# Optimization experiments

Measured on AMD Instinct MI355X. Metric: run time of the kernel, lower is better.

Reference implementation:

```python
import jax, jax.numpy as jnp
from jax import lax
import numpy as np

IMG = 512
NUM_CLASSES = 80
K_PRE = 256            # per-class pre-NMS candidates (TF combined NMS prunes similarly)
MAX_PER_CLASS = 100
MAX_TOTAL = 100
IOU_THR = 0.5
ANY_IOU_THR = 0.7
SCORE_THR = 0.05
NEG = -1e9


def make_anchors(img=IMG):
    """RetinaNet-style anchors for FPN levels 3..7, 9 per cell, [y1,x1,y2,x2]."""
    out = []
    for l in range(3, 8):
        s = 2 ** l
        n = img // s
        c = (np.arange(n) + 0.5) * s
        cy, cx = np.meshgrid(c, c, indexing='ij')
        base = 4.0 * s
        hs, ws = [], []
        for r in [0.5, 1.0, 2.0]:
            for sc in [1.0, 2 ** (1 / 3), 2 ** (2 / 3)]:
                hs.append(base * sc * np.sqrt(r))
                ws.append(base * sc / np.sqrt(r))
        hs = np.asarray(hs); ws = np.asarray(ws)  # [9]
        cy = cy[..., None]; cx = cx[..., None]
        a = np.stack([cy - hs / 2, cx - ws / 2, cy + hs / 2, cx + ws / 2], -1)  # [n,n,9,4]
        out.append(a.reshape(-1, 4))
    return np.concatenate(out, 0).astype(np.float32)


def setup_inputs() -> dict:
    key = jax.random.key(0)
    k1, k2, k3, k4 = jax.random.split(key, 4)
    anchors = jnp.asarray(make_anchors())          # [49104, 4]
    A = anchors.shape[0]
    B = 8
    # logits biased low, mimicking focal-loss bias init; few anchors fire
    y_cls = jax.random.normal(k1, (B, A, NUM_CLASSES), jnp.float32) - 4.0
    y_bbox = jax.random.normal(k2, (B, A, 4), jnp.float32) * 0.1
    orig_hs = jax.random.randint(k3, (B,), 480, 1080).astype(jnp.int32)
    orig_ws = jax.random.randint(k4, (B,), 640, 1920).astype(jnp.int32)
    return {"y_cls": y_cls, "y_bbox": y_bbox, "anchors": anchors,
            "orig_hs": orig_hs, "orig_ws": orig_ws}


def decode_boxes(anchors, rel):
    """bboxes_from_fast_rcnn: anchors [A,4], rel [B,A,4] -> [B,A,4] (y1,x1,y2,x2)."""
    ha = anchors[:, 2] - anchors[:, 0]
    wa = anchors[:, 3] - anchors[:, 1]
    cya = anchors[:, 0] + 0.5 * ha
    cxa = anchors[:, 1] + 0.5 * wa
    cy = cya + rel[..., 0] * ha
    cx = cxa + rel[..., 1] * wa
    h = ha * jnp.exp(rel[..., 2])
    w = wa * jnp.exp(rel[..., 3])
    return jnp.stack([cy - 0.5 * h, cx - 0.5 * w, cy + 0.5 * h, cx + 0.5 * w], -1)


def pairwise_iou(b):
    """[K,4] -> [K,K] IoU."""
    y1, x1, y2, x2 = b[:, 0], b[:, 1], b[:, 2], b[:, 3]
    area = (y2 - y1) * (x2 - x1)
    ih = jnp.maximum(jnp.minimum(y2[:, None], y2[None, :]) - jnp.maximum(y1[:, None], y1[None, :]), 0.0)
    iw = jnp.maximum(jnp.minimum(x2[:, None], x2[None, :]) - jnp.maximum(x1[:, None], x1[None, :]), 0.0)
    inter = ih * iw
    return inter / (area[:, None] + area[None, :] - inter + 1e-8)


def greedy_nms(boxes, valid, iou_thr, max_keep):
    """Greedy NMS over score-sorted boxes [K,4]; returns keep mask [K]."""
    K = boxes.shape[0]
    iou_m = pairwise_iou(boxes)
    ar = jnp.arange(K)

    def step(sup, i):
        k = valid[i] & jnp.logical_not(sup[i])
        sup = sup | (k & (iou_m[i] > iou_thr) & (ar > i))
        return sup, k

    _, keep = lax.scan(step, jnp.zeros(K, bool), ar)
    rank = jnp.cumsum(keep) - 1
    return keep & (rank < max_keep)


def reference(y_cls, y_bbox, anchors, orig_hs, orig_ws):
    B, A, C = y_cls.shape
    scores = jax.nn.sigmoid(y_cls)                 # [B,A,C]
    boxes = decode_boxes(anchors, y_bbox)          # [B,A,4]

    # --- per-class combined NMS ---
    st = jnp.swapaxes(scores, 1, 2)                # [B,C,A]
    top_s, top_i = lax.top_k(st, K_PRE)            # [B,C,K]
    boxes_c = jnp.take_along_axis(boxes[:, None, :, :], top_i[..., None], axis=2)  # [B,C,K,4]
    valid = top_s > SCORE_THR
    keep = jax.vmap(jax.vmap(lambda b, v: greedy_nms(b, v, IOU_THR, MAX_PER_CLASS)))(boxes_c, valid)

    masked = jnp.where(keep, top_s, NEG).reshape(B, -1)           # [B,C*K]
    cls_ids = jnp.broadcast_to(jnp.arange(C, dtype=jnp.float32)[None, :, None],
                               (B, C, K_PRE)).reshape(B, -1)
    boxes_flat = boxes_c.reshape(B, -1, 4)

    sel_s, sel_i = lax.top_k(masked, MAX_TOTAL)    # [B,T]
    sel_valid = sel_s > NEG / 2
    sel_boxes = jnp.take_along_axis(boxes_flat, sel_i[..., None], axis=1)
    sel_cls = jnp.take_along_axis(cls_ids, sel_i, axis=1)
    out_scores = jnp.where(sel_valid, sel_s, 0.0)
    out_boxes = jnp.where(sel_valid[..., None], sel_boxes, 0.0)
    out_cls = jnp.where(sel_valid, sel_cls, 0.0)
    valid_det = jnp.sum(sel_valid, axis=1).astype(jnp.int32)

    # --- resize to original image dims (bboxes_resize) ---
    rh = orig_hs.astype(jnp.float32) / IMG
    rw = orig_ws.astype(jnp.float32) / IMG
    scale = jnp.stack([rh, rw, rh, rw], -1)[:, None, :]
    lim = jnp.stack([orig_hs, orig_ws, orig_hs, orig_ws], -1).astype(jnp.float32)[:, None, :]
    rb = jnp.clip(out_boxes * scale, 0.0, lim)

    # --- class-agnostic second NMS (scores already sorted desc) ---
    v2 = jnp.arange(MAX_TOTAL)[None, :] < valid_det[:, None]
    keep2 = jax.vmap(lambda b, v: greedy_nms(b, v, ANY_IOU_THR, MAX_TOTAL))(rb, v2)

    # compact kept detections to the front (ragged gather in the original)
    perm = jnp.argsort(jnp.logical_not(keep2), axis=1, stable=True)
    fb = jnp.take_along_axis(rb, perm[..., None], axis=1)
    fs = jnp.take_along_axis(out_scores, perm, axis=1)
    fc = jnp.take_along_axis(out_cls, perm, axis=1)
    nv = jnp.sum(keep2, axis=1).astype(jnp.int32)
    m = jnp.arange(MAX_TOTAL)[None, :] < nv[:, None]
    return (jnp.where(m[..., None], fb, 0.0), jnp.where(m, fs, 0.0), jnp.where(m, fc, 0.0), nv)
```

## Files before the change

### kernel.cpp

```cpp
#include <hip/hip_runtime.h>
#include <cstdint>

#define NEGF    (-1.0e9f)
#define THR_PRE (-1.55f)
#define THR_VALID (-2.9444389791664403f)
#define CAP 512
#define FCAP 1024
#define NCLS 80
#define APB 512
#define NSH 96
#define SLOT 20
#define BCAP 512
#define KCAP 128

__device__ __forceinline__ unsigned fkey(float v){
  unsigned b = __float_as_uint(v);
  return b ^ ((b & 0x80000000u) ? 0xFFFFFFFFu : 0x80000000u);
}
__device__ __forceinline__ float fkey_inv(unsigned k){
  unsigned b = (k & 0x80000000u) ? (k ^ 0x80000000u) : ~k;
  return __uint_as_float(b);
}

template<int N, int NT>
__device__ void bitonic_desc(unsigned long long* buf){
  const int tid = threadIdx.x;
  __syncthreads();
  for (int k = 2; k <= N; k <<= 1){
    for (int j = k >> 1; j > 0; j >>= 1){
      for (int t = tid; t < N/2; t += NT){
        int i = ((t & ~(j-1)) << 1) | (t & (j-1));
        int p = i | j;
        unsigned long long a = buf[i], b = buf[p];
        bool sw = ((i & k) == 0) ? (a < b) : (a > b);
        if (sw){ buf[i] = b; buf[p] = a; }
      }
      __syncthreads();
    }
  }
}

__global__ void k_filter(const float* __restrict__ ycls, int A,
                         unsigned* __restrict__ pcnt, unsigned long long* __restrict__ pairs){
  const int b  = blockIdx.y;
  const int sh = blockIdx.x;
  const int a0 = sh * APB;
  const int tid = threadIdx.x;
  __shared__ unsigned long long s_cand[BCAP];
  __shared__ unsigned char     s_crow[BCAP];
  __shared__ unsigned s_n;
  __shared__ unsigned s_cnt[NCLS], s_cur[NCLS];
  if (tid == 0) s_n = 0;
  if (tid < NCLS){ s_cnt[tid] = 0u; s_cur[tid] = 0u; }
  __syncthreads();

  const float4* p4 = (const float4*)(ycls + ((size_t)b*A + a0)*NCLS);
  const int nval = (min(APB, A - a0)) * NCLS;
  const int n4 = nval >> 2;
  for (int t = tid; t < n4; t += blockDim.x){
    float4 v = p4[t];
    int idx  = t << 2;
    int aloc = idx / NCLS;
    int c0   = idx - aloc*NCLS;
    unsigned a = (unsigned)(a0 + aloc);
    float vv[4] = {v.x, v.y, v.z, v.w};
    #pragma unroll
    for (int j = 0; j < 4; j++){
      if (vv[j] > THR_PRE){
        unsigned s = atomicAdd(&s_n, 1u);
        if (s < BCAP){
          s_cand[s] = ((unsigned long long)fkey(vv[j]) << 32) | (unsigned)(~a);
          s_crow[s] = (unsigned char)(c0 + j);
        }
      }
    }
  }
  __syncthreads();
  unsigned n = s_n; if (n > BCAP) n = BCAP;
  for (unsigned i = tid; i < n; i += blockDim.x)
    atomicAdd(&s_cnt[s_crow[i]], 1u);
  __syncthreads();
  if (tid < NCLS){
    unsigned ccl = s_cnt[tid]; if (ccl > SLOT) ccl = SLOT;
    pcnt[(size_t)(b*NCLS + tid)*NSH + sh] = ccl;
  }
  for (unsigned i = tid; i < n; i += blockDim.x){
    int c = s_crow[i];
    unsigned off = atomicAdd(&s_cur[c], 1u);
    if (off < SLOT)
      pairs[((size_t)(b*NCLS + c)*NSH + sh)*SLOT + off] = s_cand[i];
  }
}

__global__ void k_topk_nms(const unsigned* __restrict__ pcnt, const unsigned long long* __restrict__ pairs,
                           const float* __restrict__ ycls, const float4* __restrict__ ybbox,
                           const float4* __restrict__ anchors,
                           float4* __restrict__ sbox,
                           unsigned long long* __restrict__ bcand, unsigned* __restrict__ kcnt,
                           unsigned A, unsigned C){
  const int row = blockIdx.x, tid = threadIdx.x;
  const unsigned b = (unsigned)row / C, c = (unsigned)row % C;
  __shared__ __align__(16) char smem[5120];
  unsigned long long* L = (unsigned long long*)smem;
  __shared__ unsigned sc[128];
  __shared__ unsigned s_n, s_kc;
  __shared__ unsigned long long s_K, s_keep[4];

  unsigned ct = 0;
  if (tid < 128){
    ct = (tid < NSH) ? pcnt[(size_t)row*NSH + tid] : 0u;
    sc[tid] = ct;
  }
  __syncthreads();
  #pragma unroll
  for (int d = 1; d < 128; d <<= 1){
    unsigned v = 0;
    if (tid < 128 && tid >= d) v = sc[tid - d];
    __syncthreads();
    if (tid < 128 && tid >= d) sc[tid] += v;
    __syncthreads();
  }
  unsigned n = sc[127];

  for (int i = tid; i < CAP; i += 256) L[i] = 0ull;
  __syncthreads();
  if (n >= 256u){
    if (tid < NSH && ct > 0){
      unsigned base = sc[tid] - ct;
      const unsigned long long* src = pairs + ((size_t)row*NSH + tid)*SLOT;
      for (unsigned i = 0; i < ct; ++i){
        unsigned d = base + i;
        if (d < CAP) L[d] = src[i];
      }
    }
  } else {
    if (tid == 0) s_n = 0;
    __syncthreads();
    for (unsigned aa = tid; aa < A; aa += 256){
      float v = ycls[((size_t)b*A + aa)*C + c];
      if (v > THR_VALID){
        unsigned s = atomicAdd(&s_n, 1u);
        if (s < CAP) L[s] = ((unsigned long long)fkey(v) << 32) | (unsigned)(~aa);
      }
    }
    __syncthreads();
    n = s_n;
  }
  if (n > CAP) n = CAP;
  __syncthreads();
  unsigned long long a = L[2*tid], bb = L[2*tid + 1];

  auto ce_local = [&](int k){
    bool desc = (((2*tid) & k) == 0);
    bool sw = desc ? (a < bb) : (a > bb);
    if (sw){ unsigned long long t = a; a = bb; bb = t; }
  };
  auto ce_shfl = [&](int k, int m){
    unsigned long long pa = __shfl_xor(a, m);
    unsigned long long pb = __shfl_xor(bb, m);
    bool low  = ((tid & m) == 0);
    bool desc = (((2*tid) & k) == 0);
    bool takeMax = (low == desc);
    a  = takeMax ? (a  > pa ? a  : pa) : (a  < pa ? a  : pa);
    bb = takeMax ? (bb > pb ? bb : pb) : (bb < pb ? bb : pb);
  };
  auto ce_lds = [&](int k, int j){
    L[2*tid] = a; L[2*tid + 1] = bb;
    __syncthreads();
    unsigned long long pa = L[(2*tid) ^ j];
    unsigned long long pb = L[(2*tid + 1) ^ j];
    bool lowa = (((2*tid) & j) == 0);
    bool desc = (((2*tid) & k) == 0);
    bool takeMax = (lowa == desc);
    a  = takeMax ? (a  > pa ? a  : pa) : (a  < pa ? a  : pa);
    bb = takeMax ? (bb > pb ? bb : pb) : (bb < pb ? bb : pb);
    __syncthreads();
  };

  ce_local(2);
  #pragma unroll
  for (int k = 4; k <= 128; k <<= 1){
    #pragma unroll
    for (int m = k >> 2; m >= 1; m >>= 1) ce_shfl(k, m);
    ce_local(k);
  }
  ce_lds(256, 128);
  #pragma unroll
  for (int m = 32; m >= 1; m >>= 1) ce_shfl(256, m);
  ce_local(256);
  ce_lds(512, 256);
  ce_lds(512, 128);
  #pragma unroll
  for (int m = 32; m >= 1; m >>= 1) ce_shfl(512, m);
  ce_local(512);

  if (tid < 128){ L[2*tid] = a; L[2*tid + 1] = bb; }
  __syncthreads();
  unsigned long long p = L[tid];
  __syncthreads();

  unsigned m = n < 256u ? n : 256u;
  float lg = NEGF; float4 bx = make_float4(0.f,0.f,0.f,0.f);
  if ((unsigned)tid < m){
    unsigned key  = (unsigned)(p >> 32);
    unsigned aidx = ~(unsigned)(p & 0xFFFFFFFFull);
    lg = fkey_inv(key);
    float4 an = anchors[aidx];
    float4 rl = ybbox[(size_t)b*A + aidx];
    float ha = an.z - an.x, wa = an.w - an.y;
    float cya = an.x + 0.5f*ha, cxa = an.y + 0.5f*wa;
    float cy = cya + rl.x*ha, cx = cxa + rl.y*wa;
    float h = ha * expf(rl.z), w = wa * expf(rl.w);
    bx = make_float4(cy - 0.5f*h, cx - 0.5f*w, cy + 0.5f*h, cx + 0.5f*w);
  }
  sbox[(size_t)row*256 + tid] = bx;

  float4* s_box = (float4*)smem;
  float*  s_ar  = (float*)(smem + 4096);
  float AA = (bx.z - bx.x) * (bx.w - bx.y);
  s_box[tid] = bx; s_ar[tid] = AA;
  if (tid == 0) s_kc = 0u;
  __syncthreads();

  unsigned long long M[4];
  float Y1 = bx.x, X1 = bx.y, Y2 = bx.z, X2 = bx.w;
  #pragma unroll
  for (int ch = 0; ch < 4; ++ch){
    unsigned long long mm = 0ull;
    for (int i0 = ch*64; i0 < ch*64 + 64 && i0 < tid; i0 += 4){
      #pragma unroll
      for (int k = 0; k < 4; ++k){
        int i = i0 + k;
        float4 ob = s_box[i];
        float oar = s_ar[i];
        float ih = fmaxf(fminf(Y2, ob.z) - fmaxf(Y1, ob.x), 0.f);
        float iw = fmaxf(fminf(X2, ob.w) - fmaxf(X1, ob.y), 0.f);
        float inter = ih * iw;
        float denom = AA + oar - inter + 1e-8f;
        if (inter + inter >= 0.999f * denom){
          float iou = inter / denom;
          if (iou > 0.5f && i < tid) mm |= 1ull << (i & 63);
        }
      }
    }
    M[ch] = mm;
  }

  bool valid = lg > THR_VALID;
  bool sup = false;
  #pragma unroll
  for (int ch = 0; ch < 4; ++ch){
    __syncthreads();
    if ((tid >> 6) == ch){
      unsigned long long S = __ballot(sup);
      unsigned long long V = __ballot(valid);
      unsigned long long Mcc = M[ch];
      unsigned long long kept = 0ull, keep_o = 0ull;
      unsigned kc = s_kc;
      for (int i = 0; i < 64; ++i){
        if (((V >> i) & 1ull) && !((S >> i) & 1ull)){
          if (kc < 100u) keep_o |= 1ull << i;
          kc++;
          kept |= 1ull << i;
          S |= __ballot((Mcc >> i) & 1ull);
        }
      }
      if ((tid & 63) == 0){ s_K = kept; s_keep[ch] = keep_o; s_kc = kc; }
    }
    __syncthreads();
    sup = sup || ((M[ch] & s_K) != 0ull);
  }

  const unsigned ch4 = (unsigned)tid >> 6, ln4 = (unsigned)tid & 63u;
  bool kp = (s_keep[ch4] >> ln4) & 1ull;
  if (tid == 0)
    kcnt[row] = (unsigned)(__popcll(s_keep[0]) + __popcll(s_keep[1]) +
                           __popcll(s_keep[2]) + __popcll(s_keep[3]));
  if (kp){
    unsigned pre = (unsigned)__popcll(s_keep[ch4] & ((1ull << ln4) - 1ull));
    for (unsigned k2 = 0; k2 < ch4; ++k2) pre += (unsigned)__popcll(s_keep[k2]);
    unsigned f = c*256u + (unsigned)tid;
    bcand[(size_t)row*KCAP + pre] =
      ((unsigned long long)fkey(lg) << 32) | (unsigned)(~f);
  }
}

__global__ void k_final(const unsigned long long* __restrict__ bcand, const unsigned* __restrict__ kcnt,
                        const float4* __restrict__ sbox,
                        const int* __restrict__ ohs, const int* __restrict__ ows,
                        float* __restrict__ out, int C, int B){
  const int b = blockIdx.x, tid = threadIdx.x;
  __shared__ unsigned hist[4096];
  __shared__ unsigned kc[NCLS];
  __shared__ unsigned s_total, nb, thrkey;
  __shared__ unsigned long long buf[FCAP];
  __shared__ float ry1[100],rx1[100],ry2[100],rx2[100],rar[100],rsc[100],rcl[100];
  __shared__ unsigned long long s_K2, s_keep2[2];
  __shared__ unsigned s_kc2;

  for (int i = tid; i < 4096; i += 1024) hist[i] = 0u;
  if (tid < NCLS) kc[tid] = kcnt[b*NCLS + tid];
  if (tid == 0){ s_total = 0u; nb = 0u; thrkey = 0xFFFFFFFFu; s_kc2 = 0u; }
  __syncthreads();
  if (tid < NCLS) atomicAdd(&s_total, kc[tid]);
  const unsigned long long* cb = bcand + (size_t)(b*NCLS)*KCAP;
  for (int t = tid; t < NCLS*KCAP; t += 1024){
    int cc = t >> 7, i = t & (KCAP-1);
    if ((unsigned)i < kc[cc])
      atomicAdd(&hist[(unsigned)(cb[(size_t)cc*KCAP + i] >> 32) >> 20], 1u);
  }
  __syncthreads();
  const unsigned total = s_total;

  const unsigned target = total < 100u ? total : 100u;
  if (tid < 64 && target > 0u){
    const int ln = tid;
    unsigned v = 0;
    #pragma unroll 8
    for (int i = 0; i < 64; i++) v += hist[(ln << 6) | ((i + ln) & 63)];
    #pragma unroll
    for (int d = 1; d < 64; d <<= 1){ unsigned u = __shfl_down(v, d); if (ln + d < 64) v += u; }
    unsigned long long gm = __ballot(v >= target);
    int gstar = 63 - __builtin_clzll(gm);
    unsigned ca = (gstar < 63) ? __shfl(v, gstar + 1) : 0u;
    unsigned h = hist[(gstar << 6) | ln];
    #pragma unroll
    for (int d = 1; d < 64; d <<= 1){ unsigned u = __shfl_down(h, d); if (ln + d < 64) h += u; }
    h += ca;
    unsigned long long bm = __ballot(h >= target);
    int bstar = 63 - __builtin_clzll(bm);
    if (ln == 0) thrkey = (unsigned)((gstar << 6) | bstar) << 20;
  }
  __syncthreads();
  const unsigned tk = thrkey;
  if (tk != 0xFFFFFFFFu){
    for (int t = tid; t < NCLS*KCAP; t += 1024){
      int cc = t >> 7, i = t & (KCAP-1);
      if ((unsigned)i < kc[cc]){
        unsigned long long e = cb[(size_t)cc*KCAP + i];
        if ((unsigned)(e >> 32) >= tk){
          unsigned sl = atomicAdd(&nb, 1u);
          if (sl < FCAP) buf[sl] = e;
        }
      }
    }
  }
  __syncthreads();
  unsigned nbv = nb; if (nbv > FCAP) nbv = FCAP;
  for (int i = tid; i < FCAP; i += 1024) if (i >= (int)nbv) buf[i] = 0ull;
  bitonic_desc<FCAP,1024>(buf);
  const int vd = (int)target;

  if (tid < 100){
    float e0=0,e1=0,e2=0,e3=0, s=0, cl=0;
    if (tid < vd){
      unsigned long long p = buf[tid];
      unsigned key = (unsigned)(p >> 32);
      unsigned f   = ~(unsigned)(p & 0xFFFFFFFFull);
      float lg = fkey_inv(key);
      s  = 1.0f / (1.0f + expf(-lg));
      int c = (int)(f >> 8), kk = (int)(f & 255u);
      cl = (float)c;
      float4 bx = sbox[((size_t)(b*C + c))*256 + kk];
      float oh = (float)ohs[b], ow = (float)ows[b];
      float rh = oh / 512.0f, rw = ow / 512.0f;
      e0 = fminf(fmaxf(bx.x*rh, 0.f), oh);
      e1 = fminf(fmaxf(bx.y*rw, 0.f), ow);
      e2 = fminf(fmaxf(bx.z*rh, 0.f), oh);
      e3 = fminf(fmaxf(bx.w*rw, 0.f), ow);
    }
    ry1[tid]=e0; rx1[tid]=e1; ry2[tid]=e2; rx2[tid]=e3;
    rar[tid]=(e2-e0)*(e3-e1); rsc[tid]=s; rcl[tid]=cl;
  }
  __syncthreads();

  unsigned long long M2[2] = {0ull, 0ull};
  if (tid < 100){
    float Y1=ry1[tid],X1=rx1[tid],Y2=ry2[tid],X2=rx2[tid],AA=rar[tid];
    for (int i = 0; i < tid; i++){
      float ih = fmaxf(fminf(Y2,ry2[i]) - fmaxf(Y1,ry1[i]), 0.f);
      float iw = fmaxf(fminf(X2,rx2[i]) - fmaxf(X1,rx1[i]), 0.f);
      float inter = ih*iw;
      float iou = inter / (AA + rar[i] - inter + 1e-8f);
      if (iou > 0.7f){ if (i < 64) M2[0] |= 1ull<<i; else M2[1] |= 1ull<<(i-64); }
    }
  }
  bool valid2 = tid < vd;
  bool sup2 = false;
  #pragma unroll
  for (int ch = 0; ch < 2; ++ch){
    __syncthreads();
    if ((tid >> 6) == ch){
      unsigned long long S = __ballot(sup2);
      unsigned long long V = __ballot(valid2);
      unsigned long long Mcc = M2[ch];
      unsigned long long kept = 0ull, keep_o = 0ull;
      unsigned kc2 = s_kc2;
      for (int i = 0; i < 64; ++i){
        if (((V >> i) & 1ull) && !((S >> i) & 1ull)){
          if (kc2 < 100u) keep_o |= 1ull << i;
          kc2++;
          kept |= 1ull << i;
          S |= __ballot((Mcc >> i) & 1ull);
        }
      }
      if ((tid & 63) == 0){ s_K2 = kept; s_keep2[ch] = keep_o; s_kc2 = kc2; }
    }
    __syncthreads();
    if (tid < 128) sup2 = sup2 || ((M2[ch] & s_K2) != 0ull);
  }

  float* fb  = out;
  float* fs  = out + (size_t)B*100*4;
  float* fc  = fs + (size_t)B*100;
  float* fnv = fc + (size_t)B*100;
  if (tid < 100){
    fs[b*100 + tid] = 0.f; fc[b*100 + tid] = 0.f;
    ((float4*)fb)[b*100 + tid] = make_float4(0.f,0.f,0.f,0.f);
  }
  __syncthreads();
  if (tid < 100){
    unsigned ch = (unsigned)tid >> 6, ln = (unsigned)tid & 63u;
    bool kp = (s_keep2[ch] >> ln) & 1ull;
    if (kp){
      unsigned pos = (unsigned)__popcll(s_keep2[ch] & ((1ull << ln) - 1ull));
      if (ch) pos += (unsigned)__popcll(s_keep2[0]);
      fs[b*100 + pos] = rsc[tid];
      fc[b*100 + pos] = rcl[tid];
      ((float4*)fb)[b*100 + pos] = make_float4(ry1[tid], rx1[tid], ry2[tid], rx2[tid]);
    }
  }
  if (tid == 0) fnv[b] = (float)(__popcll(s_keep2[0]) + __popcll(s_keep2[1]));
}

extern "C" void kernel_launch(void* const* d_in, const int* in_sizes, int n_in,
                              void* d_out, int out_size, void* d_ws, size_t ws_size,
                              hipStream_t stream){
  const float* ycls    = (const float*)d_in[0];
  const float* ybbox   = (const float*)d_in[1];
  const float* anchors = (const float*)d_in[2];
  const int*   ohs     = (const int*)d_in[3];
  const int*   ows     = (const int*)d_in[4];
  const int A = in_sizes[2] / 4;
  const int B = in_sizes[3];
  const int C = in_sizes[0] / (A * B);
  const int R = B * C;

  char* ws = (char*)d_ws;
  unsigned*            pcnt  = (unsigned*)ws;
  unsigned long long*  pairs = (unsigned long long*)(ws + 262144);
  float4*              sbox  = (float4*)(ws + 262144 + 9830400);
  unsigned long long*  bcand = (unsigned long long*)(ws + 262144 + 9830400 + 2621440);
  unsigned*            kcnt  = (unsigned*)(ws + 262144 + 9830400 + 2621440 + 655360);

  const int S = (A + APB - 1) / APB;
  k_filter   <<<dim3(S, B), 256, 0, stream>>>(ycls, A, pcnt, pairs);
  k_topk_nms <<<R, 256, 0, stream>>>(pcnt, pairs, ycls, (const float4*)ybbox, (const float4*)anchors,
                                     sbox, bcand, kcnt, (unsigned)A, (unsigned)C);
  k_final    <<<B, 1024, 0, stream>>>(bcand, kcnt, sbox, ohs, ows, (float*)d_out, C, B);
}
```

Measured before the change: 137.4 us.

## Fuse filter, per-class top-k NMS and final merge into one cooperative kernel

Merges the three launches into a single cooperative kernel with R=B*C blocks that uses grid-wide syncs between the filter, per-class sort/NMS and final merge phases. The filter is reshaped to 80 shards of 614 anchors per image so the grid matches the per-class row count, and it scatters candidates directly to global slots through per-class LDS atomics instead of staging them first. The final phase now runs on 256 threads with a 256-entry bitonic sort instead of 1024 threads and 1024 entries. It removes launch gaps at the cost of grid barriers, needs all 640 blocks co-resident, and may truncate if more than 256 candidates pass the threshold.

```diff
diff --git a/kernel.cpp b/kernel.cpp
--- a/kernel.cpp
+++ b/kernel.cpp
@@ -1,16 +1,18 @@
 #include <hip/hip_runtime.h>
+#include <hip/hip_cooperative_groups.h>
 #include <cstdint>
+
+namespace cg = cooperative_groups;
 
 #define NEGF    (-1.0e9f)
 #define THR_PRE (-1.55f)
 #define THR_VALID (-2.9444389791664403f)
 #define CAP 512
-#define FCAP 1024
+#define FCAP2 256
 #define NCLS 80
-#define APB 512
-#define NSH 96
-#define SLOT 20
-#define BCAP 512
+#define APB2 614
+#define NSH2 80
+#define SLOT2 26
 #define KCAP 128
 
 __device__ __forceinline__ unsigned fkey(float v){
@@ -40,422 +42,421 @@
   }
 }
 
-__global__ void k_filter(const float* __restrict__ ycls, int A,
-                         unsigned* __restrict__ pcnt, unsigned long long* __restrict__ pairs){
-  const int b  = blockIdx.y;
-  const int sh = blockIdx.x;
-  const int a0 = sh * APB;
+__global__ void __launch_bounds__(256)
+k_all(const float* __restrict__ ycls, const float4* __restrict__ ybbox,
+      const float4* __restrict__ anchors, const int* __restrict__ ohs, const int* __restrict__ ows,
+      float* __restrict__ out,
+      unsigned* __restrict__ pcnt, unsigned long long* __restrict__ pairs,
+      float4* __restrict__ sbox, unsigned long long* __restrict__ bcand, unsigned* __restrict__ kcnt,
+      int A, int C, int B){
+  cg::grid_group gg = cg::this_grid();
   const int tid = threadIdx.x;
-  __shared__ unsigned long long s_cand[BCAP];
-  __shared__ unsigned char     s_crow[BCAP];
-  __shared__ unsigned s_n;
-  __shared__ unsigned s_cnt[NCLS], s_cur[NCLS];
-  if (tid == 0) s_n = 0;
-  if (tid < NCLS){ s_cnt[tid] = 0u; s_cur[tid] = 0u; }
-  __syncthreads();
-
-  const float4* p4 = (const float4*)(ycls + ((size_t)b*A + a0)*NCLS);
-  const int nval = (min(APB, A - a0)) * NCLS;
-  const int n4 = nval >> 2;
-  for (int t = tid; t < n4; t += blockDim.x){
-    float4 v = p4[t];
-    int idx  = t << 2;
-    int aloc = idx / NCLS;
-    int c0   = idx - aloc*NCLS;
-    unsigned a = (unsigned)(a0 + aloc);
-    float vv[4] = {v.x, v.y, v.z, v.w};
-    #pragma unroll
-    for (int j = 0; j < 4; j++){
-      if (vv[j] > THR_PRE){
-        unsigned s = atomicAdd(&s_n, 1u);
-        if (s < BCAP){
-          s_cand[s] = ((unsigned long long)fkey(vv[j]) << 32) | (unsigned)(~a);
-          s_crow[s] = (unsigned char)(c0 + j);
-        }
-      }
-    }
-  }
-  __syncthreads();
-  unsigned n = s_n; if (n > BCAP) n = BCAP;
-  for (unsigned i = tid; i < n; i += blockDim.x)
-    atomicAdd(&s_cnt[s_crow[i]], 1u);
-  __syncthreads();
-  if (tid < NCLS){
-    unsigned ccl = s_cnt[tid]; if (ccl > SLOT) ccl = SLOT;
-    pcnt[(size_t)(b*NCLS + tid)*NSH + sh] = ccl;
-  }
-  for (unsigned i = tid; i < n; i += blockDim.x){
-    int c = s_crow[i];
-    unsigned off = atomicAdd(&s_cur[c], 1u);
-    if (off < SLOT)
-      pairs[((size_t)(b*NCLS + c)*NSH + sh)*SLOT + off] = s_cand[i];
-  }
-}
-
-__global__ void k_topk_nms(const unsigned* __restrict__ pcnt, const unsigned long long* __restrict__ pairs,
-                           const float* __restrict__ ycls, const float4* __restrict__ ybbox,
-                           const float4* __restrict__ anchors,
-                           float4* __restrict__ sbox,
-                           unsigned long long* __restrict__ bcand, unsigned* __restrict__ kcnt,
-                           unsigned A, unsigned C){
-  const int row = blockIdx.x, tid = threadIdx.x;
-  const unsigned b = (unsigned)row / C, c = (unsigned)row % C;
-  __shared__ __align__(16) char smem[5120];
-  unsigned long long* L = (unsigned long long*)smem;
-  __shared__ unsigned sc[128];
+  __shared__ __align__(16) char arena[21632];
   __shared__ unsigned s_n, s_kc;
   __shared__ unsigned long long s_K, s_keep[4];
 
-  unsigned ct = 0;
-  if (tid < 128){
-    ct = (tid < NSH) ? pcnt[(size_t)row*NSH + tid] : 0u;
-    sc[tid] = ct;
+  {
+    const int g  = blockIdx.x;
+    const int pb = g / NSH2;
+    const int ps = g % NSH2;
+    const int a0 = ps * APB2;
+    unsigned* s_cur = (unsigned*)arena;
+    if (tid < NCLS) s_cur[tid] = 0u;
+    __syncthreads();
+    const float4* p4 = (const float4*)(ycls + ((size_t)pb*A + a0)*NCLS);
+    const int nval = (min(APB2, A - a0)) * NCLS;
+    const int n4 = nval >> 2;
+    for (int t = tid; t < n4; t += 256){
+      float4 v = p4[t];
+      int idx  = t << 2;
+      int aloc = idx / NCLS;
+      int c0   = idx - aloc*NCLS;
+      unsigned a = (unsigned)(a0 + aloc);
+      float vv[4] = {v.x, v.y, v.z, v.w};
+      #pragma unroll
+      for (int j = 0; j < 4; j++){
+        if (vv[j] > THR_PRE){
+          int c = c0 + j;
+          unsigned off = atomicAdd(&s_cur[c], 1u);
+          if (off < SLOT2)
+            pairs[((size_t)(pb*NCLS + c)*NSH2 + ps)*SLOT2 + off] =
+              ((unsigned long long)fkey(vv[j]) << 32) | (unsigned)(~a);
+        }
+      }
+    }
+    __syncthreads();
+    if (tid < NCLS){
+      unsigned cc = s_cur[tid]; if (cc > SLOT2) cc = SLOT2;
+      pcnt[(size_t)(pb*NCLS + tid)*NSH2 + ps] = cc;
+    }
   }
-  __syncthreads();
-  #pragma unroll
-  for (int d = 1; d < 128; d <<= 1){
-    unsigned v = 0;
-    if (tid < 128 && tid >= d) v = sc[tid - d];
-    __syncthreads();
-    if (tid < 128 && tid >= d) sc[tid] += v;
-    __syncthreads();
+  __threadfence();
+  gg.sync();
+
+  {
+    const int row = blockIdx.x;
+    const unsigned b = (unsigned)row / C, c = (unsigned)row % C;
+    unsigned long long* L = (unsigned long long*)arena;
+    unsigned* sc   = (unsigned*)(arena + 4096);
+    unsigned* scnt = (unsigned*)(arena + 4608);
+
+    unsigned ct = 0;
+    if (tid < 128){
+      ct = (tid < NSH2) ? pcnt[(size_t)row*NSH2 + tid] : 0u;
+      sc[tid] = ct;
+      if (tid < NSH2) scnt[tid] = ct;
+    }
+    __syncthreads();
+    #pragma unroll
+    for (int d = 1; d < 128; d <<= 1){
+      unsigned v = 0;
+      if (tid < 128 && tid >= d) v = sc[tid - d];
+      __syncthreads();
+      if (tid < 128 && tid >= d) sc[tid] += v;
+      __syncthreads();
+    }
+    unsigned n = sc[127];
+
+    for (int i = tid; i < CAP; i += 256) L[i] = 0ull;
+    __syncthreads();
+    if (n >= 256u){
+      for (int t = tid; t < NSH2*SLOT2; t += 256){
+        int s = t / SLOT2, i = t - s*SLOT2;
+        unsigned cs = scnt[s];
+        if ((unsigned)i < cs){
+          unsigned d = sc[s] - cs + (unsigned)i;
+          if (d < CAP) L[d] = pairs[((size_t)row*NSH2 + s)*SLOT2 + i];
+        }
+      }
+    } else {
+      if (tid == 0) s_n = 0;
+      __syncthreads();
+      for (unsigned aa = tid; aa < (unsigned)A; aa += 256){
+        float v = ycls[((size_t)b*A + aa)*C + c];
+        if (v > THR_VALID){
+          unsigned s = atomicAdd(&s_n, 1u);
+          if (s < CAP) L[s] = ((unsigned long long)fkey(v) << 32) | (unsigned)(~aa);
+        }
+      }
+      __syncthreads();
+      n = s_n;
+    }
+    if (n > CAP) n = CAP;
+    __syncthreads();
+    unsigned long long a = L[2*tid], bb = L[2*tid + 1];
+
+    auto ce_local = [&](int k){
+      bool desc = (((2*tid) & k) == 0);
+      bool sw = desc ? (a < bb) : (a > bb);
+      if (sw){ unsigned long long t = a; a = bb; bb = t; }
+    };
+    auto ce_shfl = [&](int k, int m){
+      unsigned long long pa = __shfl_xor(a, m);
+      unsigned long long pb = __shfl_xor(bb, m);
+      bool low  = ((tid & m) == 0);
+      bool desc = (((2*tid) & k) == 0);
+      bool takeMax = (low == desc);
+      a  = takeMax ? (a  > pa ? a  : pa) : (a  < pa ? a  : pa);
+      bb = takeMax ? (bb > pb ? bb : pb) : (bb < pb ? bb : pb);
+    };
+    auto ce_lds = [&](int k, int j){
+      L[2*tid] = a; L[2*tid + 1] = bb;
+      __syncthreads();
+      unsigned long long pa = L[(2*tid) ^ j];
+      unsigned long long pb = L[(2*tid + 1) ^ j];
+      bool lowa = (((2*tid) & j) == 0);
+      bool desc = (((2*tid) & k) == 0);
+      bool takeMax = (lowa == desc);
+      a  = takeMax ? (a  > pa ? a  : pa) : (a  < pa ? a  : pa);
+      bb = takeMax ? (bb > pb ? bb : pb) : (bb < pb ? bb : pb);
+      __syncthreads();
+    };
+
+    ce_local(2);
+    #pragma unroll
+    for (int k = 4; k <= 128; k <<= 1){
+      #pragma unroll
+      for (int m = k >> 2; m >= 1; m >>= 1) ce_shfl(k, m);
+      ce_local(k);
+    }
+    ce_lds(256, 128);
+    #pragma unroll
+    for (int m = 32; m >= 1; m >>= 1) ce_shfl(256, m);
+    ce_local(256);
+    ce_lds(512, 256);
+    ce_lds(512, 128);
+    #pragma unroll
+    for (int m = 32; m >= 1; m >>= 1) ce_shfl(512, m);
+    ce_local(512);
+
+    if (tid < 128){ L[2*tid] = a; L[2*tid + 1] = bb; }
+    __syncthreads();
+    unsigned long long p = L[tid];
+    __syncthreads();
+
+    unsigned m = n < 256u ? n : 256u;
+    float lg = NEGF; float4 bx = make_float4(0.f,0.f,0.f,0.f);
+    if ((unsigned)tid < m){
+      unsigned key  = (unsigned)(p >> 32);
+      unsigned aidx = ~(unsigned)(p & 0xFFFFFFFFull);
+      lg = fkey_inv(key);
+      float4 an = anchors[aidx];
+      float4 rl = ybbox[(size_t)b*A + aidx];
+      float ha = an.z - an.x, wa = an.w - an.y;
+      float cya = an.x + 0.5f*ha, cxa = an.y + 0.5f*wa;
+      float cy = cya + rl.x*ha, cx = cxa + rl.y*wa;
+      float h = ha * expf(rl.z), w = wa * expf(rl.w);
+      bx = make_float4(cy - 0.5f*h, cx - 0.5f*w, cy + 0.5f*h, cx + 0.5f*w);
+    }
+    sbox[(size_t)row*256 + tid] = bx;
+
+    float4* s_box = (float4*)arena;
+    float*  s_ar  = (float*)(arena + 4096);
+    float AA = (bx.z - bx.x) * (bx.w - bx.y);
+    s_box[tid] = bx; s_ar[tid] = AA;
+    if (tid == 0) s_kc = 0u;
+    __syncthreads();
+
+    unsigned long long M[4];
+    float Y1 = bx.x, X1 = bx.y, Y2 = bx.z, X2 = bx.w;
+    #pragma unroll
+    for (int ch = 0; ch < 4; ++ch){
+      unsigned long long mm = 0ull;
+      for (int i0 = ch*64; i0 < ch*64 + 64 && i0 < tid; i0 += 4){
+        #pragma unroll
+        for (int k = 0; k < 4; ++k){
+          int i = i0 + k;
+          float4 ob = s_box[i];
+          float oar = s_ar[i];
+          float ih = fmaxf(fminf(Y2, ob.z) - fmaxf(Y1, ob.x), 0.f);
+          float iw = fmaxf(fminf(X2, ob.w) - fmaxf(X1, ob.y), 0.f);
+          float inter = ih * iw;
+          float denom = AA + oar - inter + 1e-8f;
+          if (inter + inter >= 0.999f * denom){
+            float iou = inter / denom;
+            if (iou > 0.5f && i < tid) mm |= 1ull << (i & 63);
+          }
+        }
+      }
+      M[ch] = mm;
+    }
+
+    bool valid = lg > THR_VALID;
+    bool sup = false;
+    #pragma unroll
+    for (int ch = 0; ch < 4; ++ch){
+      __syncthreads();
+      if ((tid >> 6) == ch){
+        unsigned long long S = __ballot(sup);
+        unsigned long long V = __ballot(valid);
+        unsigned long long Mcc = M[ch];
+        unsigned long long kept = 0ull, keep_o = 0ull;
+        unsigned kc = s_kc;
+        for (int i = 0; i < 64; ++i){
+          if (((V >> i) & 1ull) && !((S >> i) & 1ull)){
+            if (kc < 100u) keep_o |= 1ull << i;
+            kc++;
+            kept |= 1ull << i;
+            S |= __ballot((Mcc >> i) & 1ull);
+          }
+        }
+        if ((tid & 63) == 0){ s_K = kept; s_keep[ch] = keep_o; s_kc = kc; }
+      }
+      __syncthreads();
+      sup = sup || ((M[ch] & s_K) != 0ull);
+    }
+
+    const unsigned ch4 = (unsigned)tid >> 6, ln4 = (unsigned)tid & 63u;
+    bool kp = (s_keep[ch4] >> ln4) & 1ull;
+    if (tid == 0)
+      kcnt[row] = (unsigned)(__popcll(s_keep[0]) + __popcll(s_keep[1]) +
+                             __popcll(s_keep[2]) + __popcll(s_keep[3]));
+    if (kp){
+      unsigned pre = (unsigned)__popcll(s_keep[ch4] & ((1ull << ln4) - 1ull));
+      for (unsigned k2 = 0; k2 < ch4; ++k2) pre += (unsigned)__popcll(s_keep[k2]);
+      unsigned f = c*256u + (unsigned)tid;
+      bcand[(size_t)row*KCAP + pre] =
+        ((unsigned long long)fkey(lg) << 32) | (unsigned)(~f);
+    }
   }
-  unsigned n = sc[127];
-
-  for (int i = tid; i < CAP; i += 256) L[i] = 0ull;
-  __syncthreads();
-  if (n >= 256u){
-    if (tid < NSH && ct > 0){
-      unsigned base = sc[tid] - ct;
-      const unsigned long long* src = pairs + ((size_t)row*NSH + tid)*SLOT;
-      for (unsigned i = 0; i < ct; ++i){
-        unsigned d = base + i;
-        if (d < CAP) L[d] = src[i];
-      }
-    }
-  } else {
-    if (tid == 0) s_n = 0;
-    __syncthreads();
-    for (unsigned aa = tid; aa < A; aa += 256){
-      float v = ycls[((size_t)b*A + aa)*C + c];
-      if (v > THR_VALID){
-        unsigned s = atomicAdd(&s_n, 1u);
-        if (s < CAP) L[s] = ((unsigned long long)fkey(v) << 32) | (unsigned)(~aa);
-      }
-    }
-    __syncthreads();
-    n = s_n;
+  __threadfence();
+  gg.sync();
+
+  if (blockIdx.x >= B) return;
+  {
+    const int b = blockIdx.x;
+    unsigned* hist = (unsigned*)arena;
+    unsigned long long* buf = (unsigned long long*)(arena + 16384);
+    float* ry1 = (float*)(arena + 18432);
+    float* rx1 = (float*)(arena + 18832);
+    float* ry2 = (float*)(arena + 19232);
+    float* rx2 = (float*)(arena + 19632);
+    float* rar = (float*)(arena + 20032);
+    float* rsc = (float*)(arena + 20432);
+    float* rcl = (float*)(arena + 20832);
+    unsigned* kcl = (unsigned*)(arena + 21232);
+    __shared__ unsigned s_total, nb, thrkey, s_kc2;
+    __shared__ unsigned long long s_K2, s_keep2[2];
+
+    for (int i = tid; i < 4096; i += 256) hist[i] = 0u;
+    if (tid < NCLS) kcl[tid] = kcnt[b*NCLS + tid];
+    if (tid == 0){ s_total = 0u; nb = 0u; thrkey = 0xFFFFFFFFu; s_kc2 = 0u; }
+    __syncthreads();
+    if (tid < NCLS) atomicAdd(&s_total, kcl[tid]);
+    const unsigned long long* cb = bcand + (size_t)(b*NCLS)*KCAP;
+    for (int t = tid; t < NCLS*KCAP; t += 256){
+      int cc = t >> 7, i = t & (KCAP-1);
+      if ((unsigned)i < kcl[cc])
+        atomicAdd(&hist[(unsigned)(cb[(size_t)cc*KCAP + i] >> 32) >> 20], 1u);
+    }
+    __syncthreads();
+    const unsigned total = s_total;
+
+    const unsigned target = total < 100u ? total : 100u;
+    if (tid < 64 && target > 0u){
+      const int ln = tid;
+      unsigned v = 0;
+      #pragma unroll 8
+      for (int i = 0; i < 64; i++) v += hist[(ln << 6) | ((i + ln) & 63)];
+      #pragma unroll
+      for (int d = 1; d < 64; d <<= 1){ unsigned u = __shfl_down(v, d); if (ln + d < 64) v += u; }
+      unsigned long long gm = __ballot(v >= target);
+      int gstar = 63 - __builtin_clzll(gm);
+      unsigned ca = (gstar < 63) ? __shfl(v, gstar + 1) : 0u;
+      unsigned h = hist[(gstar << 6) | ln];
+      #pragma unroll
+      for (int d = 1; d < 64; d <<= 1){ unsigned u = __shfl_down(h, d); if (ln + d < 64) h += u; }
+      h += ca;
+      unsigned long long bm = __ballot(h >= target);
+      int bstar = 63 - __builtin_clzll(bm);
+      if (ln == 0) thrkey = (unsigned)((gstar << 6) | bstar) << 20;
+    }
+    __syncthreads();
+    const unsigned tk = thrkey;
+    if (tk != 0xFFFFFFFFu){
+      for (int t = tid; t < NCLS*KCAP; t += 256){
+        int cc = t >> 7, i = t & (KCAP-1);
+        if ((unsigned)i < kcl[cc]){
+          unsigned long long e = cb[(size_t)cc*KCAP + i];
+          if ((unsigned)(e >> 32) >= tk){
+            unsigned sl = atomicAdd(&nb, 1u);
+            if (sl < FCAP2) buf[sl] = e;
+          }
+        }
+      }
+    }
+    __syncthreads();
+    unsigned nbv = nb; if (nbv > FCAP2) nbv = FCAP2;
+    if (tid < FCAP2 && (unsigned)tid >= nbv) buf[tid] = 0ull;
+    bitonic_desc<FCAP2,256>(buf);
+    const int vd = (int)target;
+
+    if (tid < 100){
+      float e0=0,e1=0,e2=0,e3=0, s=0, cl=0;
+      if (tid < vd){
+        unsigned long long p = buf[tid];
+        unsigned key = (unsigned)(p >> 32);
+        unsigned f   = ~(unsigned)(p & 0xFFFFFFFFull);
+        float lg = fkey_inv(key);
+        s  = 1.0f / (1.0f + expf(-lg));
+        int c = (int)(f >> 8), kk = (int)(f & 255u);
+        cl = (float)c;
+        float4 bx = sbox[((size_t)(b*C + c))*256 + kk];
+        float oh = (float)ohs[b], ow = (float)ows[b];
+        float rh = oh / 512.0f, rw = ow / 512.0f;
+        e0 = fminf(fmaxf(bx.x*rh, 0.f), oh);
+        e1 = fminf(fmaxf(bx.y*rw, 0.f), ow);
+        e2 = fminf(fmaxf(bx.z*rh, 0.f), oh);
+        e3 = fminf(fmaxf(bx.w*rw, 0.f), ow);
+      }
+      ry1[tid]=e0; rx1[tid]=e1; ry2[tid]=e2; rx2[tid]=e3;
+      rar[tid]=(e2-e0)*(e3-e1); rsc[tid]=s; rcl[tid]=cl;
+    }
+    __syncthreads();
+
+    unsigned long long M2[2] = {0ull, 0ull};
+    if (tid < 100){
+      float Y1=ry1[tid],X1=rx1[tid],Y2=ry2[tid],X2=rx2[tid],AA=rar[tid];
+      for (int i = 0; i < tid; i++){
+        float ih = fmaxf(fminf(Y2,ry2[i]) - fmaxf(Y1,ry1[i]), 0.f);
+        float iw = fmaxf(fminf(X2,rx2[i]) - fmaxf(X1,rx1[i]), 0.f);
+        float inter = ih*iw;
+        float iou = inter / (AA + rar[i] - inter + 1e-8f);
+        if (iou > 0.7f){ if (i < 64) M2[0] |= 1ull<<i; else M2[1] |= 1ull<<(i-64); }
+      }
+    }
+    bool valid2 = tid < vd;
+    bool sup2 = false;
+    #pragma unroll
+    for (int ch = 0; ch < 2; ++ch){
+      __syncthreads();
+      if ((tid >> 6) == ch){
+        unsigned long long S = __ballot(sup2);
+        unsigned long long V = __ballot(valid2);
+        unsigned long long Mcc = M2[ch];
+        unsigned long long kept = 0ull, keep_o = 0ull;
+        unsigned kc2 = s_kc2;
+        for (int i = 0; i < 64; ++i){
+          if (((V >> i) & 1ull) && !((S >> i) & 1ull)){
+            if (kc2 < 100u) keep_o |= 1ull << i;
+            kc2++;
+            kept |= 1ull << i;
+            S |= __ballot((Mcc >> i) & 1ull);
+          }
+        }
+        if ((tid & 63) == 0){ s_K2 = kept; s_keep2[ch] = keep_o; s_kc2 = kc2; }
+      }
+      __syncthreads();
+      if (tid < 128) sup2 = sup2 || ((M2[ch] & s_K2) != 0ull);
+    }
+
+    float* fb  = out;
+    float* fs  = out + (size_t)B*100*4;
+    float* fc  = fs + (size_t)B*100;
+    float* fnv = fc + (size_t)B*100;
+    if (tid < 100){
+      fs[b*100 + tid] = 0.f; fc[b*100 + tid] = 0.f;
+      ((float4*)fb)[b*100 + tid] = make_float4(0.f,0.f,0.f,0.f);
+    }
+    __syncthreads();
+    if (tid < 100){
+      unsigned ch = (unsigned)tid >> 6, ln = (unsigned)tid & 63u;
+      bool kp = (s_keep2[ch] >> ln) & 1ull;
+      if (kp){
+        unsigned pos = (unsigned)__popcll(s_keep2[ch] & ((1ull << ln) - 1ull));
+        if (ch) pos += (unsigned)__popcll(s_keep2[0]);
+        fs[b*100 + pos] = rsc[tid];
+        fc[b*100 + pos] = rcl[tid];
+        ((float4*)fb)[b*100 + pos] = make_float4(ry1[tid], rx1[tid], ry2[tid], rx2[tid]);
+      }
+    }
+    if (tid == 0) fnv[b] = (float)(__popcll(s_keep2[0]) + __popcll(s_keep2[1]));
   }
-  if (n > CAP) n = CAP;
-  __syncthreads();
-  unsigned long long a = L[2*tid], bb = L[2*tid + 1];
-
-  auto ce_local = [&](int k){
-    bool desc = (((2*tid) & k) == 0);
-    bool sw = desc ? (a < bb) : (a > bb);
-    if (sw){ unsigned long long t = a; a = bb; bb = t; }
-  };
-  auto ce_shfl = [&](int k, int m){
-    unsigned long long pa = __shfl_xor(a, m);
-    unsigned long long pb = __shfl_xor(bb, m);
-    bool low  = ((tid & m) == 0);
-    bool desc = (((2*tid) & k) == 0);
-    bool takeMax = (low == desc);
-    a  = takeMax ? (a  > pa ? a  : pa) : (a  < pa ? a  : pa);
-    bb = takeMax ? (bb > pb ? bb : pb) : (bb < pb ? bb : pb);
-  };
-  auto ce_lds = [&](int k, int j){
-    L[2*tid] = a; L[2*tid + 1] = bb;
-    __syncthreads();
-    unsigned long long pa = L[(2*tid) ^ j];
-    unsigned long long pb = L[(2*tid + 1) ^ j];
-    bool lowa = (((2*tid) & j) == 0);
-    bool desc = (((2*tid) & k) == 0);
-    bool takeMax = (lowa == desc);
-    a  = takeMax ? (a  > pa ? a  : pa) : (a  < pa ? a  : pa);
-    bb = takeMax ? (bb > pb ? bb : pb) : (bb < pb ? bb : pb);
-    __syncthreads();
-  };
-
-  ce_local(2);
-  #pragma unroll
-  for (int k = 4; k <= 128; k <<= 1){
-    #pragma unroll
-    for (int m = k >> 2; m >= 1; m >>= 1) ce_shfl(k, m);
-    ce_local(k);
-  }
-  ce_lds(256, 128);
-  #pragma unroll
-  for (int m = 32; m >= 1; m >>= 1) ce_shfl(256, m);
-  ce_local(256);
-  ce_lds(512, 256);
-  ce_lds(512, 128);
-  #pragma unroll
-  for (int m = 32; m >= 1; m >>= 1) ce_shfl(512, m);
-  ce_local(512);
-
-  if (tid < 128){ L[2*tid] = a; L[2*tid + 1] = bb; }
-  __syncthreads();
-  unsigned long long p = L[tid];
-  __syncthreads();
-
-  unsigned m = n < 256u ? n : 256u;
-  float lg = NEGF; float4 bx = make_float4(0.f,0.f,0.f,0.f);
-  if ((unsigned)tid < m){
-    unsigned key  = (unsigned)(p >> 32);
-    unsigned aidx = ~(unsigned)(p & 0xFFFFFFFFull);
-    lg = fkey_inv(key);
-    float4 an = anchors[aidx];
-    float4 rl = ybbox[(size_t)b*A + aidx];
-    float ha = an.z - an.x, wa = an.w - an.y;
-    float cya = an.x + 0.5f*ha, cxa = an.y + 0.5f*wa;
-    float cy = cya + rl.x*ha, cx = cxa + rl.y*wa;
-    float h = ha * expf(rl.z), w = wa * expf(rl.w);
-    bx = make_float4(cy - 0.5f*h, cx - 0.5f*w, cy + 0.5f*h, cx + 0.5f*w);
-  }
-  sbox[(size_t)row*256 + tid] = bx;
-
-  float4* s_box = (float4*)smem;
-  float*  s_ar  = (float*)(smem + 4096);
-  float AA = (bx.z - bx.x) * (bx.w - bx.y);
-  s_box[tid] = bx; s_ar[tid] = AA;
-  if (tid == 0) s_kc = 0u;
-  __syncthreads();
-
-  unsigned long long M[4];
-  float Y1 = bx.x, X1 = bx.y, Y2 = bx.z, X2 = bx.w;
-  #pragma unroll
-  for (int ch = 0; ch < 4; ++ch){
-    unsigned long long mm = 0ull;
-    for (int i0 = ch*64; i0 < ch*64 + 64 && i0 < tid; i0 += 4){
-      #pragma unroll
-      for (int k = 0; k < 4; ++k){
-        int i = i0 + k;
-        float4 ob = s_box[i];
-        float oar = s_ar[i];
-        float ih = fmaxf(fminf(Y2, ob.z) - fmaxf(Y1, ob.x), 0.f);
-        float iw = fmaxf(fminf(X2, ob.w) - fmaxf(X1, ob.y), 0.f);
-        float inter = ih * iw;
-        float denom = AA + oar - inter + 1e-8f;
-        if (inter + inter >= 0.999f * denom){
-          float iou = inter / denom;
-          if (iou > 0.5f && i < tid) mm |= 1ull << (i & 63);
-        }
-      }
-    }
-    M[ch] = mm;
-  }
-
-  bool valid = lg > THR_VALID;
-  bool sup = false;
-  #pragma unroll
-  for (int ch = 0; ch < 4; ++ch){
-    __syncthreads();
-    if ((tid >> 6) == ch){
-      unsigned long long S = __ballot(sup);
-      unsigned long long V = __ballot(valid);
-      unsigned long long Mcc = M[ch];
-      unsigned long long kept = 0ull, keep_o = 0ull;
-      unsigned kc = s_kc;
-      for (int i = 0; i < 64; ++i){
-        if (((V >> i) & 1ull) && !((S >> i) & 1ull)){
-          if (kc < 100u) keep_o |= 1ull << i;
-          kc++;
-          kept |= 1ull << i;
-          S |= __ballot((Mcc >> i) & 1ull);
-        }
-      }
-      if ((tid & 63) == 0){ s_K = kept; s_keep[ch] = keep_o; s_kc = kc; }
-    }
-    __syncthreads();
-    sup = sup || ((M[ch] & s_K) != 0ull);
-  }
-
-  const unsigned ch4 = (unsigned)tid >> 6, ln4 = (unsigned)tid & 63u;
-  bool kp = (s_keep[ch4] >> ln4) & 1ull;
-  if (tid == 0)
-    kcnt[row] = (unsigned)(__popcll(s_keep[0]) + __popcll(s_keep[1]) +
-                           __popcll(s_keep[2]) + __popcll(s_keep[3]));
-  if (kp){
-    unsigned pre = (unsigned)__popcll(s_keep[ch4] & ((1ull << ln4) - 1ull));
-    for (unsigned k2 = 0; k2 < ch4; ++k2) pre += (unsigned)__popcll(s_keep[k2]);
-    unsigned f = c*256u + (unsigned)tid;
-    bcand[(size_t)row*KCAP + pre] =
-      ((unsigned long long)fkey(lg) << 32) | (unsigned)(~f);
-  }
-}
-
-__global__ void k_final(const unsigned long long* __restrict__ bcand, const unsigned* __restrict__ kcnt,
-                        const float4* __restrict__ sbox,
-                        const int* __restrict__ ohs, const int* __restrict__ ows,
-                        float* __restrict__ out, int C, int B){
-  const int b = blockIdx.x, tid = threadIdx.x;
-  __shared__ unsigned hist[4096];
-  __shared__ unsigned kc[NCLS];
-  __shared__ unsigned s_total, nb, thrkey;
-  __shared__ unsigned long long buf[FCAP];
-  __shared__ float ry1[100],rx1[100],ry2[100],rx2[100],rar[100],rsc[100],rcl[100];
-  __shared__ unsigned long long s_K2, s_keep2[2];
-  __shared__ unsigned s_kc2;
-
-  for (int i = tid; i < 4096; i += 1024) hist[i] = 0u;
-  if (tid < NCLS) kc[tid] = kcnt[b*NCLS + tid];
-  if (tid == 0){ s_total = 0u; nb = 0u; thrkey = 0xFFFFFFFFu; s_kc2 = 0u; }
-  __syncthreads();
-  if (tid < NCLS) atomicAdd(&s_total, kc[tid]);
-  const unsigned long long* cb = bcand + (size_t)(b*NCLS)*KCAP;
-  for (int t = tid; t < NCLS*KCAP; t += 1024){
-    int cc = t >> 7, i = t & (KCAP-1);
-    if ((unsigned)i < kc[cc])
-      atomicAdd(&hist[(unsigned)(cb[(size_t)cc*KCAP + i] >> 32) >> 20], 1u);
-  }
-  __syncthreads();
-  const unsigned total = s_total;
-
-  const unsigned target = total < 100u ? total : 100u;
-  if (tid < 64 && target > 0u){
-    const int ln = tid;
-    unsigned v = 0;
-    #pragma unroll 8
-    for (int i = 0; i < 64; i++) v += hist[(ln << 6) | ((i + ln) & 63)];
-    #pragma unroll
-    for (int d = 1; d < 64; d <<= 1){ unsigned u = __shfl_down(v, d); if (ln + d < 64) v += u; }
-    unsigned long long gm = __ballot(v >= target);
-    int gstar = 63 - __builtin_clzll(gm);
-    unsigned ca = (gstar < 63) ? __shfl(v, gstar + 1) : 0u;
-    unsigned h = hist[(gstar << 6) | ln];
-    #pragma unroll
-    for (int d = 1; d < 64; d <<= 1){ unsigned u = __shfl_down(h, d); if (ln + d < 64) h += u; }
-    h += ca;
-    unsigned long long bm = __ballot(h >= target);
-    int bstar = 63 - __builtin_clzll(bm);
-    if (ln == 0) thrkey = (unsigned)((gstar << 6) | bstar) << 20;
-  }
-  __syncthreads();
-  const unsigned tk = thrkey;
-  if (tk != 0xFFFFFFFFu){
-    for (int t = tid; t < NCLS*KCAP; t += 1024){
-      int cc = t >> 7, i = t & (KCAP-1);
-      if ((unsigned)i < kc[cc]){
-        unsigned long long e = cb[(size_t)cc*KCAP + i];
-        if ((unsigned)(e >> 32) >= tk){
-          unsigned sl = atomicAdd(&nb, 1u);
-          if (sl < FCAP) buf[sl] = e;
-        }
-      }
-    }
-  }
-  __syncthreads();
-  unsigned nbv = nb; if (nbv > FCAP) nbv = FCAP;
-  for (int i = tid; i < FCAP; i += 1024) if (i >= (int)nbv) buf[i] = 0ull;
-  bitonic_desc<FCAP,1024>(buf);
-  const int vd = (int)target;
-
-  if (tid < 100){
-    float e0=0,e1=0,e2=0,e3=0, s=0, cl=0;
-    if (tid < vd){
-      unsigned long long p = buf[tid];
-      unsigned key = (unsigned)(p >> 32);
-      unsigned f   = ~(unsigned)(p & 0xFFFFFFFFull);
-      float lg = fkey_inv(key);
-      s  = 1.0f / (1.0f + expf(-lg));
-      int c = (int)(f >> 8), kk = (int)(f & 255u);
-      cl = (float)c;
-      float4 bx = sbox[((size_t)(b*C + c))*256 + kk];
-      float oh = (float)ohs[b], ow = (float)ows[b];
-      float rh = oh / 512.0f, rw = ow / 512.0f;
-      e0 = fminf(fmaxf(bx.x*rh, 0.f), oh);
-      e1 = fminf(fmaxf(bx.y*rw, 0.f), ow);
-      e2 = fminf(fmaxf(bx.z*rh, 0.f), oh);
-      e3 = fminf(fmaxf(bx.w*rw, 0.f), ow);
-    }
-    ry1[tid]=e0; rx1[tid]=e1; ry2[tid]=e2; rx2[tid]=e3;
-    rar[tid]=(e2-e0)*(e3-e1); rsc[tid]=s; rcl[tid]=cl;
-  }
-  __syncthreads();
-
-  unsigned long long M2[2] = {0ull, 0ull};
-  if (tid < 100){
-    float Y1=ry1[tid],X1=rx1[tid],Y2=ry2[tid],X2=rx2[tid],AA=rar[tid];
-    for (int i = 0; i < tid; i++){
-      float ih = fmaxf(fminf(Y2,ry2[i]) - fmaxf(Y1,ry1[i]), 0.f);
-      float iw = fmaxf(fminf(X2,rx2[i]) - fmaxf(X1,rx1[i]), 0.f);
-      float inter = ih*iw;
-      float iou = inter / (AA + rar[i] - inter + 1e-8f);
-      if (iou > 0.7f){ if (i < 64) M2[0] |= 1ull<<i; else M2[1] |= 1ull<<(i-64); }
-    }
-  }
-  bool valid2 = tid < vd;
-  bool sup2 = false;
-  #pragma unroll
-  for (int ch = 0; ch < 2; ++ch){
-    __syncthreads();
-    if ((tid >> 6) == ch){
-      unsigned long long S = __ballot(sup2);
-      unsigned long long V = __ballot(valid2);
-      unsigned long long Mcc = M2[ch];
-      unsigned long long kept = 0ull, keep_o = 0ull;
-      unsigned kc2 = s_kc2;
-      for (int i = 0; i < 64; ++i){
-        if (((V >> i) & 1ull) && !((S >> i) & 1ull)){
-          if (kc2 < 100u) keep_o |= 1ull << i;
-          kc2++;
-          kept |= 1ull << i;
-          S |= __ballot((Mcc >> i) & 1ull);
-        }
-      }
-      if ((tid & 63) == 0){ s_K2 = kept; s_keep2[ch] = keep_o; s_kc2 = kc2; }
-    }
-    __syncthreads();
-    if (tid < 128) sup2 = sup2 || ((M2[ch] & s_K2) != 0ull);
-  }
-
-  float* fb  = out;
-  float* fs  = out + (size_t)B*100*4;
-  float* fc  = fs + (size_t)B*100;
-  float* fnv = fc + (size_t)B*100;
-  if (tid < 100){
-    fs[b*100 + tid] = 0.f; fc[b*100 + tid] = 0.f;
-    ((float4*)fb)[b*100 + tid] = make_float4(0.f,0.f,0.f,0.f);
-  }
-  __syncthreads();
-  if (tid < 100){
-    unsigned ch = (unsigned)tid >> 6, ln = (unsigned)tid & 63u;
-    bool kp = (s_keep2[ch] >> ln) & 1ull;
-    if (kp){
-      unsigned pos = (unsigned)__popcll(s_keep2[ch] & ((1ull << ln) - 1ull));
-      if (ch) pos += (unsigned)__popcll(s_keep2[0]);
-      fs[b*100 + pos] = rsc[tid];
-      fc[b*100 + pos] = rcl[tid];
-      ((float4*)fb)[b*100 + pos] = make_float4(ry1[tid], rx1[tid], ry2[tid], rx2[tid]);
-    }
-  }
-  if (tid == 0) fnv[b] = (float)(__popcll(s_keep2[0]) + __popcll(s_keep2[1]));
 }
 
 extern "C" void kernel_launch(void* const* d_in, const int* in_sizes, int n_in,
                               void* d_out, int out_size, void* d_ws, size_t ws_size,
                               hipStream_t stream){
-  const float* ycls    = (const float*)d_in[0];
-  const float* ybbox   = (const float*)d_in[1];
-  const float* anchors = (const float*)d_in[2];
-  const int*   ohs     = (const int*)d_in[3];
-  const int*   ows     = (const int*)d_in[4];
-  const int A = in_sizes[2] / 4;
-  const int B = in_sizes[3];
-  const int C = in_sizes[0] / (A * B);
+  const float*  ycls    = (const float*)d_in[0];
+  const float4* ybbox   = (const float4*)d_in[1];
+  const float4* anchors = (const float4*)d_in[2];
+  const int*    ohs     = (const int*)d_in[3];
+  const int*    ows     = (const int*)d_in[4];
+  int A = in_sizes[2] / 4;
+  int B = in_sizes[3];
+  int C = in_sizes[0] / (A * B);
   const int R = B * C;
 
   char* ws = (char*)d_ws;
-  unsigned*            pcnt  = (unsigned*)ws;
-  unsigned long long*  pairs = (unsigned long long*)(ws + 262144);
-  float4*              sbox  = (float4*)(ws + 262144 + 9830400);
-  unsigned long long*  bcand = (unsigned long long*)(ws + 262144 + 9830400 + 2621440);
-  unsigned*            kcnt  = (unsigned*)(ws + 262144 + 9830400 + 2621440 + 655360);
-
-  const int S = (A + APB - 1) / APB;
-  k_filter   <<<dim3(S, B), 256, 0, stream>>>(ycls, A, pcnt, pairs);
-  k_topk_nms <<<R, 256, 0, stream>>>(pcnt, pairs, ycls, (const float4*)ybbox, (const float4*)anchors,
-                                     sbox, bcand, kcnt, (unsigned)A, (unsigned)C);
-  k_final    <<<B, 1024, 0, stream>>>(bcand, kcnt, sbox, ohs, ows, (float*)d_out, C, B);
+  unsigned*           pcnt  = (unsigned*)ws;
+  unsigned long long* pairs = (unsigned long long*)(ws + 262144);
+  float4*             sbox  = (float4*)(ws + 262144 + 10747904);
+  unsigned long long* bcand = (unsigned long long*)(ws + 262144 + 10747904 + 2621440);
+  unsigned*           kcnt  = (unsigned*)(ws + 262144 + 10747904 + 2621440 + 655360);
+  float*              outp  = (float*)d_out;
+
+  void* args[] = { (void*)&ycls, (void*)&ybbox, (void*)&anchors, (void*)&ohs, (void*)&ows,
+                   (void*)&outp, (void*)&pcnt, (void*)&pairs, (void*)&sbox, (void*)&bcand,
+                   (void*)&kcnt, (void*)&A, (void*)&C, (void*)&B };
+  hipLaunchCooperativeKernel((const void*)k_all, dim3(R), dim3(256), args, 0, stream);
 }
```

Result: slower. 381.2 us (+177.5%).
